# Kernel optimization log

Measured on AMD Instinct MI355X. Metric: run time of the kernel, lower is better.

## Reference

```python
import jax, jax.numpy as jnp
import numpy as np

MEM = 8          # memory_length
DEG = 5          # degree
WDIM = 1 + DEG * MEM  # 41
B, L = 32, 4096


def setup_inputs() -> dict:
    key = jax.random.key(0)
    k1, k2, k3 = jax.random.split(key, 3)
    x = jax.random.normal(k1, (B, L, 2), dtype=jnp.float32)
    h_0 = jnp.zeros((B, MEM), dtype=jnp.float32)
    # xavier-ish init of the complex weight, kept as two real tensors
    Wreal = jax.random.normal(k2, (MEM, WDIM), dtype=jnp.float32) * 0.05
    Wimag = jax.random.normal(k3, (MEM, WDIM), dtype=jnp.float32) * 0.05
    return {"x": x, "h_0": h_0, "Wreal": Wreal, "Wimag": Wimag}


def reference(x, h_0, Wreal, Wimag):
    Bb, Ll, _ = x.shape
    M, D = MEM, DEG
    Weight = jax.lax.complex(Wreal, Wimag)              # (M, W) complex64
    xc = jax.lax.complex(x[..., 0], x[..., 1])          # (B, L)
    xc = jnp.concatenate([jnp.zeros((Bb, 2 * M - 1), xc.dtype), xc], axis=1)  # (B, S), S=L+2M-1
    amp = jnp.abs(xc)                                    # (B, S) real
    # channel 0: complex signal; channels 1..D: amp**(i) for i=0..D-1 (cast to complex)
    ch = jnp.stack([xc] + [(amp ** i).astype(xc.dtype) for i in range(D)], axis=0)  # (D+1, B, S)
    # sliding windows of length M: num_frames = S - M + 1 = L + M
    idx = jnp.arange(Ll + M)[:, None] + jnp.arange(M)[None, :]  # (L+M, M)
    chw = ch[:, :, idx]                                  # (D+1, B, L+M, M)
    base = chw[0, :, :Ll, :]                             # (B, L, M): x window at frame j
    # cross term for feature w = 1 + m*D + d is base * window(channel d, frame j+m)
    # NOTE: d indexes channels 0..D-1, so d=0 uses the complex signal channel (as in the torch code)
    shifts = jnp.stack([chw[:D, :, m:m + Ll, :] for m in range(M)], axis=0)  # (M, D, B, L, M)
    cross = base[None, None] * shifts                    # (M, D, B, L, Mwin)
    cross = jnp.moveaxis(cross.reshape(M * D, Bb, Ll, M), 0, -1)  # (B, L, Mwin, M*D)
    F = jnp.concatenate([base[..., None], cross], axis=-1)        # (B, L, M, W)
    # original sums over batch AND (M, W): one complex scalar per frame j
    co = jnp.einsum('bjkw,kw->j', F, Weight)             # (L,) complex
    out = jnp.stack([co.real, co.imag], axis=-1)         # (L, 2)
    return jnp.broadcast_to(out[None], (Bb, Ll, 2)).astype(jnp.float32)
```

## Files before the change

kernel.cpp:

```cpp
#include <hip/hip_runtime.h>
#include <math.h>

#define MEMN 8
#define WDIM 41
#define BB   32
#define LL   4096
#define PADN 15
#define TILE_T 8
#define WIN 22
#define STRIDE 23


__global__ __launch_bounds__(256)
void gmp_kernel(const float* __restrict__ x,
                const float* __restrict__ Wr,
                const float* __restrict__ Wi,
                float* __restrict__ out)
{
    __shared__ float s_re[BB * STRIDE];
    __shared__ float s_im[BB * STRIDE];
    __shared__ float s_am[BB * STRIDE];
    __shared__ float s_co[TILE_T][2];

    const int tid = threadIdx.x;
    const int t0  = blockIdx.x * TILE_T;

    {
        const int o  = tid & 31;
        const int b8 = tid >> 5;
        if (o < WIN) {
            const int g = t0 - PADN + o;
            #pragma unroll
            for (int it = 0; it < 4; ++it) {
                const int b = b8 + 8 * it;
                float re = 0.f, im = 0.f;
                if (g >= 0) {
                    const float2 v = *(const float2*)(x + ((size_t)b * LL + g) * 2);
                    re = v.x; im = v.y;
                }
                s_re[b * STRIDE + o] = re;
                s_im[b * STRIDE + o] = im;
                s_am[b * STRIDE + o] = sqrtf(re * re + im * im);
            }
        }
    }
    __syncthreads();

    const int b    = tid & 31;
    const int slot = tid >> 5;
    const int base = b * STRIDE + slot;

    float zr[15], zi[15], a1[15], a2[15], a3[15];
    #pragma unroll
    for (int k = 0; k < 15; ++k) {
        zr[k] = s_re[base + k];
        zi[k] = s_im[base + k];
        a1[k] = s_am[base + k];
        a2[k] = a1[k] * a1[k];
        a3[k] = a2[k] * a1[k];
    }

    float cr = 0.f, ci = 0.f;
    #pragma unroll
    for (int m = 0; m < MEMN; ++m) {
        float ar = Wr[m * WDIM];
        float ai = Wi[m * WDIM];
        #pragma unroll
        for (int mm = 0; mm < MEMN; ++mm) {
            const int k  = m + mm;
            const int wb = m * WDIM + 1 + 5 * mm;
            const float w0r = Wr[wb], w0i = Wi[wb];
            ar += w0r * zr[k] - w0i * zi[k];
            ai += w0r * zi[k] + w0i * zr[k];
            ar += Wr[wb + 1] + Wr[wb + 2] * a1[k] + Wr[wb + 3] * a2[k] + Wr[wb + 4] * a3[k];
            ai += Wi[wb + 1] + Wi[wb + 2] * a1[k] + Wi[wb + 3] * a2[k] + Wi[wb + 4] * a3[k];
        }
        cr += zr[m] * ar - zi[m] * ai;
        ci += zr[m] * ai + zi[m] * ar;
    }

    #pragma unroll
    for (int mask = 16; mask >= 1; mask >>= 1) {
        cr += __shfl_xor(cr, mask, 64);
        ci += __shfl_xor(ci, mask, 64);
    }
    if (b == 0) {
        s_co[slot][0] = cr;
        s_co[slot][1] = ci;
    }
    __syncthreads();

    const int bw = tid >> 3;
    const int j  = tid & 7;
    float2 v;
    v.x = s_co[j][0];
    v.y = s_co[j][1];
    *(float2*)(out + ((size_t)bw * LL + t0 + j) * 2) = v;
}

extern "C" void kernel_launch(void* const* d_in, const int* in_sizes, int n_in,
                              void* d_out, int out_size, void* d_ws, size_t ws_size,
                              hipStream_t stream) {
    const float* x  = (const float*)d_in[0];
    const float* Wr = (const float*)d_in[2];
    const float* Wi = (const float*)d_in[3];
    float* out = (float*)d_out;

    gmp_kernel<<<dim3(LL / TILE_T), dim3(256), 0, stream>>>(x, Wr, Wi, out);
}
```

Before: 68.94 us.

## Split memory taps across thread groups with smaller time tiles and 512 threads

```diff
diff --git a/kernel.cpp b/kernel.cpp
--- a/kernel.cpp
+++ b/kernel.cpp
@@ -6,12 +6,12 @@
 #define BB   32
 #define LL   4096
 #define PADN 15
-#define TILE_T 8
-#define WIN 22
-#define STRIDE 23
+#define TILE_T 4
+#define WIN 18
+#define STRIDE 19
 
 
-__global__ __launch_bounds__(256)
+__global__ __launch_bounds__(512, 8)
 void gmp_kernel(const float* __restrict__ x,
                 const float* __restrict__ Wr,
                 const float* __restrict__ Wi,
@@ -20,7 +20,7 @@
     __shared__ float s_re[BB * STRIDE];
     __shared__ float s_im[BB * STRIDE];
     __shared__ float s_am[BB * STRIDE];
-    __shared__ float s_co[TILE_T][2];
+    __shared__ float s_part[TILE_T][4][2];
 
     const int tid = threadIdx.x;
     const int t0  = blockIdx.x * TILE_T;
@@ -31,8 +31,8 @@
         if (o < WIN) {
             const int g = t0 - PADN + o;
             #pragma unroll
-            for (int it = 0; it < 4; ++it) {
-                const int b = b8 + 8 * it;
+            for (int it = 0; it < 2; ++it) {
+                const int b = b8 + 16 * it;
                 float re = 0.f, im = 0.f;
                 if (g >= 0) {
                     const float2 v = *(const float2*)(x + ((size_t)b * LL + g) * 2);
@@ -47,36 +47,39 @@
     __syncthreads();
 
     const int b    = tid & 31;
-    const int slot = tid >> 5;
-    const int base = b * STRIDE + slot;
+    const int slot = (tid >> 5) & 3;
+    const int mq   = tid >> 7;
+    const int base = b * STRIDE + slot + 2 * mq;
 
-    float zr[15], zi[15], a1[15], a2[15], a3[15];
+    float zr[9], zi[9], a1[9];
     #pragma unroll
-    for (int k = 0; k < 15; ++k) {
+    for (int k = 0; k < 9; ++k) {
         zr[k] = s_re[base + k];
         zi[k] = s_im[base + k];
         a1[k] = s_am[base + k];
-        a2[k] = a1[k] * a1[k];
-        a3[k] = a2[k] * a1[k];
     }
 
     float cr = 0.f, ci = 0.f;
     #pragma unroll
-    for (int m = 0; m < MEMN; ++m) {
+    for (int ml = 0; ml < 2; ++ml) {
+        const int m = 2 * mq + ml;
         float ar = Wr[m * WDIM];
         float ai = Wi[m * WDIM];
         #pragma unroll
         for (int mm = 0; mm < MEMN; ++mm) {
-            const int k  = m + mm;
+            const int k  = ml + mm;
             const int wb = m * WDIM + 1 + 5 * mm;
             const float w0r = Wr[wb], w0i = Wi[wb];
+            const float v1 = a1[k];
+            const float v2 = v1 * v1;
+            const float v3 = v2 * v1;
             ar += w0r * zr[k] - w0i * zi[k];
             ai += w0r * zi[k] + w0i * zr[k];
-            ar += Wr[wb + 1] + Wr[wb + 2] * a1[k] + Wr[wb + 3] * a2[k] + Wr[wb + 4] * a3[k];
-            ai += Wi[wb + 1] + Wi[wb + 2] * a1[k] + Wi[wb + 3] * a2[k] + Wi[wb + 4] * a3[k];
+            ar += Wr[wb + 1] + Wr[wb + 2] * v1 + Wr[wb + 3] * v2 + Wr[wb + 4] * v3;
+            ai += Wi[wb + 1] + Wi[wb + 2] * v1 + Wi[wb + 3] * v2 + Wi[wb + 4] * v3;
         }
-        cr += zr[m] * ar - zi[m] * ai;
-        ci += zr[m] * ai + zi[m] * ar;
+        cr += zr[ml] * ar - zi[ml] * ai;
+        ci += zr[ml] * ai + zi[ml] * ar;
     }
 
     #pragma unroll
@@ -85,17 +88,19 @@
         ci += __shfl_xor(ci, mask, 64);
     }
     if (b == 0) {
-        s_co[slot][0] = cr;
-        s_co[slot][1] = ci;
+        s_part[slot][mq][0] = cr;
+        s_part[slot][mq][1] = ci;
     }
     __syncthreads();
 
-    const int bw = tid >> 3;
-    const int j  = tid & 7;
-    float2 v;
-    v.x = s_co[j][0];
-    v.y = s_co[j][1];
-    *(float2*)(out + ((size_t)bw * LL + t0 + j) * 2) = v;
+    if (tid < BB * TILE_T) {
+        const int j  = tid & (TILE_T - 1);
+        const int bw = tid >> 2;
+        float2 v;
+        v.x = s_part[j][0][0] + s_part[j][1][0] + s_part[j][2][0] + s_part[j][3][0];
+        v.y = s_part[j][0][1] + s_part[j][1][1] + s_part[j][2][1] + s_part[j][3][1];
+        *(float2*)(out + ((size_t)bw * LL + t0 + j) * 2) = v;
+    }
 }
 
 extern "C" void kernel_launch(void* const* d_in, const int* in_sizes, int n_in,
@@ -106,5 +111,5 @@
     const float* Wi = (const float*)d_in[3];
     float* out = (float*)d_out;
 
-    gmp_kernel<<<dim3(LL / TILE_T), dim3(256), 0, stream>>>(x, Wr, Wi, out);
+    gmp_kernel<<<dim3(LL / TILE_T), dim3(512), 0, stream>>>(x, Wr, Wi, out);
 }
```

Result: slower. 114.2 us (+65.7%).
